# Kernel optimization log

Hardware: AMD Instinct MI355X
Metric: run time of the kernel (lower is better)

## Reference

```python
import jax, jax.numpy as jnp
import numpy as np

B, N, M, K = 8, 24000, 6000, 32
C_IN, C_MID, C_OUT = 64, 128, 256  # channels=[64,128,256]; conv input is C_IN+3 (dp_fj)


def setup_inputs() -> dict:
    key = jax.random.key(0)
    ks = jax.random.split(key, 8)
    return {
        "query_xyz": jax.random.normal(ks[0], (B, M, 3), jnp.float32),
        "support_xyz": jax.random.normal(ks[1], (B, N, 3), jnp.float32),
        "features": jax.random.normal(ks[2], (B, C_IN, N), jnp.float32),
        "neighbor_idx": jax.random.randint(ks[3], (B, M, K), 0, N, dtype=jnp.int32),
        "W1": jax.random.normal(ks[4], (C_MID, C_IN + 3), jnp.float32) * 0.05,
        "b1": jnp.zeros((C_MID,), jnp.float32),
        "W2": jax.random.normal(ks[5], (C_OUT, C_MID), jnp.float32) * 0.05,
        "b2": jnp.zeros((C_OUT,), jnp.float32),
    }


def _conv1d_relu(x, W, b):
    # pointwise conv1d (kernel size 1) + bias + ReLU; x: [B, Cin, N]
    return jax.nn.relu(jnp.einsum('oc,bcn->bon', W, x) + b[None, :, None])


def reference(query_xyz, support_xyz, features, neighbor_idx, W1, b1, W2, b2):
    # Delayed aggregation: transform features FIRST (convs on support points),
    # then gather neighbors per query and max-reduce.
    x = jnp.concatenate([features, support_xyz.transpose(0, 2, 1)], axis=1)  # [B, C_IN+3, N]
    x = _conv1d_relu(x, W1, b1)   # [B, C_MID, N]
    x = _conv1d_relu(x, W2, b2)   # [B, C_OUT, N]
    # grouper: gather neighbor features fj = x[b, :, neighbor_idx[b, m, k]] -> [B, C_OUT, M, K]
    idx = jnp.broadcast_to(neighbor_idx.reshape(B, 1, M * K), (B, C_OUT, M * K))
    fj = jnp.take_along_axis(x, idx, axis=2).reshape(B, C_OUT, M, K)
    # reduction_layer: max over neighbor dim
    return jnp.max(fj, axis=-1)  # [B, C_OUT, M]
```

## Files before the change

kernel.cpp:

```cpp
#include <hip/hip_runtime.h>

typedef unsigned short u16;
typedef short s16x8 __attribute__((ext_vector_type(8)));
typedef float f32x4 __attribute__((ext_vector_type(4)));
typedef unsigned short u16x8 __attribute__((ext_vector_type(8)));

#define B_   8
#define N_   24000
#define M_   6000
#define K_   32
#define CIN  64
#define CMID 128
#define COUT 256
#define KP1  96
#define QB_  188

__device__ __align__(16) u16 g_W1f[CMID * KP1];
__device__ __align__(16) u16 g_W2f[COUT * CMID];
__device__ __align__(16) u16 g_Yf[(size_t)B_ * N_ * COUT];

__device__ __forceinline__ float bf2f(u16 u) {
    return __uint_as_float(((unsigned)u) << 16);
}
__device__ __forceinline__ u16 f2bf(float f) {
    unsigned u = __float_as_uint(f);
    u += 0x7FFFu + ((u >> 16) & 1u);
    return (u16)(u >> 16);
}

__global__ void prep_weights(const float* __restrict__ W1,
                             const float* __restrict__ W2) {
    int t = blockIdx.x * 256 + threadIdx.x;
    if (t < CMID * KP1) {
        int blk = t >> 9, off = t & 511;
        int L = off >> 3, j = off & 7;
        int ln = L & 15, quad = L >> 4;
        int w = blk / 6, r = blk % 6;
        int k0i = r >> 1, mt = r & 1;
        int row = w * 32 + mt * 16 + ln;
        int col = k0i * 32 + quad * 8 + j;
        g_W1f[t] = (col < 67) ? f2bf(W1[row * 67 + col]) : (u16)0;
    } else {
        int i = t - CMID * KP1;
        int blk = i >> 9, off = i & 511;
        int L = off >> 3, j = off & 7;
        int ln = L & 15, quad = L >> 4;
        int w = blk >> 4, r = blk & 15;
        int k0i = r >> 2, mt = r & 3;
        int row = w * 64 + mt * 16 + ln;
        int col = k0i * 32 + quad * 8 + j;
        g_W2f[i] = f2bf(W2[row * 128 + col]);
    }
}

__global__ __launch_bounds__(256) void conv_fused(
        const float* __restrict__ feat, const float* __restrict__ xyz,
        const float* __restrict__ b1,  const float* __restrict__ b2) {
    __shared__ __align__(16) u16 sm[16896];
    u16* Xs = sm;
    u16* Hs = sm + 6656;
    u16* Ys = sm;

    const int tid  = threadIdx.x;
    const int b    = blockIdx.y;
    const int n0   = blockIdx.x * 64;
    const int w    = tid >> 6;
    const int L    = tid & 63;
    const int ln   = L & 15;
    const int quad = L >> 4;

    if (tid < 64) {
        uint4 z; z.x = z.y = z.z = z.w = 0u;
        u16* xr = Xs + tid * 104;
        *(uint4*)(xr + 64) = z; *(uint4*)(xr + 72) = z;
        *(uint4*)(xr + 80) = z; *(uint4*)(xr + 88) = z;
        const float* s = xyz + (size_t)(b * N_ + n0 + tid) * 3;
        xr[64] = f2bf(s[0]); xr[65] = f2bf(s[1]); xr[66] = f2bf(s[2]);
    }
#pragma unroll
    for (int it = 0; it < 4; ++it) {
        int idx = it * 256 + tid;
        int c   = idx >> 4;
        int p0  = (idx & 15) << 2;
        float4 v = *(const float4*)(feat + (size_t)(b * CIN + c) * N_ + n0 + p0);
        u16* dst = Xs + p0 * 104 + c;
        dst[0]   = f2bf(v.x);
        dst[104] = f2bf(v.y);
        dst[208] = f2bf(v.z);
        dst[312] = f2bf(v.w);
    }
    __syncthreads();

    f32x4 acc1[2][4];
#pragma unroll
    for (int mt = 0; mt < 2; ++mt)
#pragma unroll
        for (int nt = 0; nt < 4; ++nt) {
            f32x4 zz = {0.f, 0.f, 0.f, 0.f};
            acc1[mt][nt] = zz;
        }
#pragma unroll
    for (int k0i = 0; k0i < 3; ++k0i) {
        s16x8 af[2], xf[4];
#pragma unroll
        for (int mt = 0; mt < 2; ++mt)
            af[mt] = *(const s16x8*)(g_W1f + (((w * 3 + k0i) * 2 + mt) << 9) + L * 8);
#pragma unroll
        for (int nt = 0; nt < 4; ++nt)
            xf[nt] = *(const s16x8*)(Xs + (nt * 16 + ln) * 104 + k0i * 32 + quad * 8);
#pragma unroll
        for (int mt = 0; mt < 2; ++mt)
#pragma unroll
            for (int nt = 0; nt < 4; ++nt)
                acc1[mt][nt] = __builtin_amdgcn_mfma_f32_16x16x32_bf16(
                    af[mt], xf[nt], acc1[mt][nt], 0, 0, 0);
    }
#pragma unroll
    for (int mt = 0; mt < 2; ++mt) {
        int m0 = w * 32 + mt * 16 + quad * 4;
        float4 bv = *(const float4*)(b1 + m0);
#pragma unroll
        for (int nt = 0; nt < 4; ++nt) {
            int p = nt * 16 + ln;
            float x0 = acc1[mt][nt][0] + bv.x;
            float x1 = acc1[mt][nt][1] + bv.y;
            float x2 = acc1[mt][nt][2] + bv.z;
            float x3 = acc1[mt][nt][3] + bv.w;
            ushort4 hv;
            hv.x = f2bf(x0 > 0.f ? x0 : 0.f);
            hv.y = f2bf(x1 > 0.f ? x1 : 0.f);
            hv.z = f2bf(x2 > 0.f ? x2 : 0.f);
            hv.w = f2bf(x3 > 0.f ? x3 : 0.f);
            *(ushort4*)(Hs + p * 136 + m0) = hv;
        }
    }
    __syncthreads();

    f32x4 acc2[4][4];
#pragma unroll
    for (int mt = 0; mt < 4; ++mt)
#pragma unroll
        for (int nt = 0; nt < 4; ++nt) {
            f32x4 zz = {0.f, 0.f, 0.f, 0.f};
            acc2[mt][nt] = zz;
        }
#pragma unroll
    for (int k0i = 0; k0i < 4; ++k0i) {
        s16x8 af[4], hf[4];
#pragma unroll
        for (int mt = 0; mt < 4; ++mt)
            af[mt] = *(const s16x8*)(g_W2f + (((w * 4 + k0i) * 4 + mt) << 9) + L * 8);
#pragma unroll
        for (int nt = 0; nt < 4; ++nt)
            hf[nt] = *(const s16x8*)(Hs + (nt * 16 + ln) * 136 + k0i * 32 + quad * 8);
#pragma unroll
        for (int mt = 0; mt < 4; ++mt)
#pragma unroll
            for (int nt = 0; nt < 4; ++nt)
                acc2[mt][nt] = __builtin_amdgcn_mfma_f32_16x16x32_bf16(
                    af[mt], hf[nt], acc2[mt][nt], 0, 0, 0);
    }
    __syncthreads();

#pragma unroll
    for (int mt = 0; mt < 4; ++mt) {
        int c0 = w * 64 + mt * 16 + quad * 4;
        float4 bv = *(const float4*)(b2 + c0);
#pragma unroll
        for (int nt = 0; nt < 4; ++nt) {
            int p = nt * 16 + ln;
            float x0 = acc2[mt][nt][0] + bv.x;
            float x1 = acc2[mt][nt][1] + bv.y;
            float x2 = acc2[mt][nt][2] + bv.z;
            float x3 = acc2[mt][nt][3] + bv.w;
            ushort4 yv;
            yv.x = f2bf(x0 > 0.f ? x0 : 0.f);
            yv.y = f2bf(x1 > 0.f ? x1 : 0.f);
            yv.z = f2bf(x2 > 0.f ? x2 : 0.f);
            yv.w = f2bf(x3 > 0.f ? x3 : 0.f);
            *(ushort4*)(Ys + p * 264 + c0) = yv;
        }
    }
    __syncthreads();

    u16* dstY = g_Yf + ((size_t)b * N_ + n0) * COUT;
#pragma unroll
    for (int i = 0; i < 8; ++i) {
        int g = i * 256 + tid;
        int p = g >> 5, c16 = g & 31;
        *(uint4*)(dstY + (size_t)p * COUT + c16 * 8) =
            *(const uint4*)(Ys + p * 264 + c16 * 8);
    }
}

__global__ __launch_bounds__(256) void gather_max(
        const int* __restrict__ nbr, float* __restrict__ out) {
    __shared__ __align__(16) int sidx[32 * K_];
    __shared__ __align__(16) u16 ymax[32 * 400];

    const int tid = threadIdx.x;
    const int l   = blockIdx.x;
    const int xcd = l & 7;
    const int j   = l >> 3;
    const int cw  = j / QB_;
    const int qb  = j % QB_;
    const int combo = cw * 8 + xcd;
    const int b   = combo >> 2;
    const int q   = combo & 3;
    const int m0  = qb * 32;

    if (m0 + (tid >> 3) < M_)
        *(int4*)(sidx + tid * 4) =
            *(const int4*)(nbr + ((size_t)b * M_ + m0) * K_ + tid * 4);
    __syncthreads();

    const int w  = tid >> 6;
    const int L  = tid & 63;
    const int kg = L >> 3;
    const int co = L & 7;
    const u16* base = g_Yf + (size_t)b * N_ * COUT + q * 64 + co * 8;

    u16x8 mx[8];
#pragma unroll
    for (int i = 0; i < 8; ++i)
        mx[i] = (u16x8){0, 0, 0, 0, 0, 0, 0, 0};

#pragma unroll
    for (int nh = 0; nh < 2; ++nh) {
        const unsigned lo = nh ? (unsigned)(N_ / 2) : 0u;
        const unsigned hi = lo + (unsigned)(N_ / 2);
#pragma unroll
        for (int i = 0; i < 8; ++i) {
            int ml = w * 8 + i;
            if (m0 + ml < M_) {
                int id[4];
#pragma unroll
                for (int r = 0; r < 4; ++r)
                    id[r] = sidx[ml * K_ + r * 8 + kg];
                u16x8 v[4];
#pragma unroll
                for (int r = 0; r < 4; ++r) {
                    unsigned u = (unsigned)id[r];
                    u = u < (unsigned)N_ ? u : 0u;
                    if (u >= lo && u < hi)
                        v[r] = *(const u16x8*)(base + (size_t)u * COUT);
                    else
                        v[r] = (u16x8){0, 0, 0, 0, 0, 0, 0, 0};
                }
                u16x8 a = __builtin_elementwise_max(v[0], v[1]);
                u16x8 c = __builtin_elementwise_max(v[2], v[3]);
                mx[i] = __builtin_elementwise_max(
                    mx[i], __builtin_elementwise_max(a, c));
            }
        }
    }

#pragma unroll
    for (int i = 0; i < 8; ++i) {
        int ml = w * 8 + i;
        if (m0 + ml < M_) {
            u16x8 m8 = mx[i];
#pragma unroll
            for (int mask = 8; mask <= 32; mask <<= 1) {
                int4 t = *(int4*)&m8;
                t.x = __shfl_xor(t.x, mask);
                t.y = __shfl_xor(t.y, mask);
                t.z = __shfl_xor(t.z, mask);
                t.w = __shfl_xor(t.w, mask);
                m8 = __builtin_elementwise_max(m8, *(u16x8*)&t);
            }
            if (kg == 0)
                *(u16x8*)(ymax + ml * 400 + co * 8) = m8;
        }
    }
    __syncthreads();

    int valid = M_ - m0; if (valid > 32) valid = 32;
#pragma unroll
    for (int it = 0; it < 2; ++it) {
        int c  = it * 32 + (tid >> 3);
        int mc = (tid & 7) << 2;
        if (mc + 4 <= valid) {
            float4 v;
            v.x = bf2f(ymax[(mc + 0) * 400 + c]);
            v.y = bf2f(ymax[(mc + 1) * 400 + c]);
            v.z = bf2f(ymax[(mc + 2) * 400 + c]);
            v.w = bf2f(ymax[(mc + 3) * 400 + c]);
            *(float4*)(out + (size_t)(b * COUT + q * 64 + c) * M_ + m0 + mc) = v;
        }
    }
}

extern "C" void kernel_launch(void* const* d_in, const int* in_sizes, int n_in,
                              void* d_out, int out_size, void* d_ws, size_t ws_size,
                              hipStream_t stream) {
    const float* xyz  = (const float*)d_in[1];
    const float* feat = (const float*)d_in[2];
    const int*   nbr  = (const int*)d_in[3];
    const float* W1   = (const float*)d_in[4];
    const float* b1   = (const float*)d_in[5];
    const float* W2   = (const float*)d_in[6];
    const float* b2   = (const float*)d_in[7];
    float* out = (float*)d_out;
    (void)d_ws; (void)ws_size;

    prep_weights<<<176, 256, 0, stream>>>(W1, W2);
    conv_fused<<<dim3(N_ / 64, B_), 256, 0, stream>>>(feat, xyz, b1, b2);
    gather_max<<<32 * QB_, 256, 0, stream>>>(nbr, out);
}
```

Before: 257.0 us.

## Bucket neighbor indices by support-point range before gather to cut wasted loads

The gather kernel now counting-sorts each query's 32 neighbor indices in shared memory into three ranges of the support set (by idx>>13). It then loads features range by range, so each pass only touches an L2-sized slice of the feature table. Previously it made two masked passes over all indices and still issued loads for out-of-range entries. The change adds shared-memory atomics, extra barriers and a variable-length inner loop, and reuses one shared buffer for indices, sorted indices and the output staging.

```diff
diff --git a/kernel.cpp b/kernel.cpp
--- a/kernel.cpp
+++ b/kernel.cpp
@@ -195,8 +195,12 @@
 
 __global__ __launch_bounds__(256) void gather_max(
         const int* __restrict__ nbr, float* __restrict__ out) {
-    __shared__ __align__(16) int sidx[32 * K_];
-    __shared__ __align__(16) u16 ymax[32 * 400];
+    __shared__ __align__(16) u16 smem[32 * 400];
+    int* sidx  = (int*)smem;
+    u16* ssort = smem + 2048;
+    int* soff  = (int*)(smem + 3072);
+    int* scur  = (int*)(smem + 3328);
+    u16* ymax  = smem;
 
     const int tid = threadIdx.x;
     const int l   = blockIdx.x;
@@ -208,10 +212,45 @@
     const int b   = combo >> 2;
     const int q   = combo & 3;
     const int m0  = qb * 32;
-
-    if (m0 + (tid >> 3) < M_)
+    const int row = tid >> 3;
+    const int Mv0 = M_ - m0;
+    const int Mv  = Mv0 < 32 ? Mv0 : 32;
+
+    if (row < Mv)
         *(int4*)(sidx + tid * 4) =
             *(const int4*)(nbr + ((size_t)b * M_ + m0) * K_ + tid * 4);
+    if (tid < 128) scur[tid] = 0;
+    __syncthreads();
+
+    unsigned uu[4];
+#pragma unroll
+    for (int jj = 0; jj < 4; ++jj) {
+        unsigned u = (unsigned)sidx[tid * 4 + jj];
+        u = u < (unsigned)N_ ? u : 0u;
+        uu[jj] = u;
+        int p = (int)(u >> 13);
+        if (p < 2) atomicAdd(&scur[row * 4 + p], 1);
+    }
+    __syncthreads();
+
+    if (tid < 32) {
+        int c0 = scur[tid * 4 + 0], c1 = scur[tid * 4 + 1];
+        soff[tid * 4 + 0] = 0;
+        soff[tid * 4 + 1] = c0;
+        soff[tid * 4 + 2] = c0 + c1;
+        soff[tid * 4 + 3] = 32;
+        scur[tid * 4 + 0] = 0;
+        scur[tid * 4 + 1] = c0;
+        scur[tid * 4 + 2] = c0 + c1;
+    }
+    __syncthreads();
+
+#pragma unroll
+    for (int jj = 0; jj < 4; ++jj) {
+        int p = (int)(uu[jj] >> 13);
+        int pos = atomicAdd(&scur[row * 4 + p], 1);
+        ssort[row * 32 + pos] = (u16)uu[jj];
+    }
     __syncthreads();
 
     const int w  = tid >> 6;
@@ -226,39 +265,51 @@
         mx[i] = (u16x8){0, 0, 0, 0, 0, 0, 0, 0};
 
 #pragma unroll
-    for (int nh = 0; nh < 2; ++nh) {
-        const unsigned lo = nh ? (unsigned)(N_ / 2) : 0u;
-        const unsigned hi = lo + (unsigned)(N_ / 2);
-#pragma unroll
-        for (int i = 0; i < 8; ++i) {
-            int ml = w * 8 + i;
-            if (m0 + ml < M_) {
-                int id[4];
-#pragma unroll
-                for (int r = 0; r < 4; ++r)
-                    id[r] = sidx[ml * K_ + r * 8 + kg];
-                u16x8 v[4];
-#pragma unroll
-                for (int r = 0; r < 4; ++r) {
-                    unsigned u = (unsigned)id[r];
-                    u = u < (unsigned)N_ ? u : 0u;
-                    if (u >= lo && u < hi)
-                        v[r] = *(const u16x8*)(base + (size_t)u * COUT);
-                    else
-                        v[r] = (u16x8){0, 0, 0, 0, 0, 0, 0, 0};
+    for (int p = 0; p < 3; ++p) {
+#pragma unroll
+        for (int h = 0; h < 2; ++h) {
+            int mq[4], beg[4], end[4], last[4];
+            u16x8 va[4], vb[4];
+#pragma unroll
+            for (int s = 0; s < 4; ++s) {
+                int ml = w * 8 + h * 4 + s;
+                mq[s]  = ml < Mv ? ml : 0;
+                beg[s] = soff[mq[s] * 4 + p];
+                end[s] = soff[mq[s] * 4 + p + 1];
+                int lt = end[s] - 1;
+                last[s] = lt > 0 ? lt : 0;
+                int p0 = beg[s] + kg; p0 = p0 < last[s] ? p0 : last[s];
+                unsigned i0 = (unsigned)ssort[mq[s] * 32 + p0];
+                va[s] = *(const u16x8*)(base + (size_t)i0 * COUT);
+            }
+#pragma unroll
+            for (int s = 0; s < 4; ++s) {
+                int p1 = beg[s] + 8 + kg; p1 = p1 < last[s] ? p1 : last[s];
+                unsigned i1 = (unsigned)ssort[mq[s] * 32 + p1];
+                vb[s] = *(const u16x8*)(base + (size_t)i1 * COUT);
+            }
+#pragma unroll
+            for (int s = 0; s < 4; ++s)
+                mx[h * 4 + s] = __builtin_elementwise_max(mx[h * 4 + s],
+                    __builtin_elementwise_max(va[s], vb[s]));
+#pragma unroll
+            for (int s = 0; s < 4; ++s) {
+                for (int r = beg[s] + 16; r < end[s]; r += 8) {
+                    int pp = r + kg; pp = pp < last[s] ? pp : last[s];
+                    unsigned ii = (unsigned)ssort[mq[s] * 32 + pp];
+                    u16x8 vv = *(const u16x8*)(base + (size_t)ii * COUT);
+                    mx[h * 4 + s] = __builtin_elementwise_max(mx[h * 4 + s], vv);
                 }
-                u16x8 a = __builtin_elementwise_max(v[0], v[1]);
-                u16x8 c = __builtin_elementwise_max(v[2], v[3]);
-                mx[i] = __builtin_elementwise_max(
-                    mx[i], __builtin_elementwise_max(a, c));
             }
         }
     }
+
+    __syncthreads();
 
 #pragma unroll
     for (int i = 0; i < 8; ++i) {
         int ml = w * 8 + i;
-        if (m0 + ml < M_) {
+        if (ml < Mv) {
             u16x8 m8 = mx[i];
 #pragma unroll
             for (int mask = 8; mask <= 32; mask <<= 1) {
@@ -275,7 +326,7 @@
     }
     __syncthreads();
 
-    int valid = M_ - m0; if (valid > 32) valid = 32;
+    int valid = Mv;
 #pragma unroll
     for (int it = 0; it < 2; ++it) {
         int c  = it * 32 + (tid >> 3);
```

Result: no change. 255.8 us (-0.5%).

## Loop gather_max over four batch/channel combos per block and drop N-half split

Applied to the files above, without the earlier changes.

The gather_max grid shrinks 4x. Each block now iterates over four (batch, channel-quarter) combos within its XCD slot, reusing the block and aliasing the index and result shared buffers. The two-pass split over halves of N, which filtered indices by range and doubled the index reads and compares, is removed so each neighbor row is loaded once. Launch bounds now request 6 blocks per CU, which may limit registers. The extra barriers per iteration and fewer blocks could reduce latency hiding, and losing the N-half split may hurt L2 locality.

```diff
diff --git a/kernel.cpp b/kernel.cpp
--- a/kernel.cpp
+++ b/kernel.cpp
@@ -193,46 +193,48 @@
     }
 }
 
-__global__ __launch_bounds__(256) void gather_max(
+__global__ __launch_bounds__(256, 6) void gather_max(
         const int* __restrict__ nbr, float* __restrict__ out) {
-    __shared__ __align__(16) int sidx[32 * K_];
-    __shared__ __align__(16) u16 ymax[32 * 400];
+    __shared__ __align__(16) u16 smem[32 * 400];
+    int* sidx = (int*)smem;
+    u16* ymax = smem;
 
     const int tid = threadIdx.x;
     const int l   = blockIdx.x;
     const int xcd = l & 7;
-    const int j   = l >> 3;
-    const int cw  = j / QB_;
-    const int qb  = j % QB_;
-    const int combo = cw * 8 + xcd;
-    const int b   = combo >> 2;
-    const int q   = combo & 3;
+    const int qb  = l >> 3;
     const int m0  = qb * 32;
-
-    if (m0 + (tid >> 3) < M_)
-        *(int4*)(sidx + tid * 4) =
-            *(const int4*)(nbr + ((size_t)b * M_ + m0) * K_ + tid * 4);
-    __syncthreads();
+    const int row = tid >> 3;
+    const int Mv0 = M_ - m0;
+    const int Mv  = Mv0 < 32 ? Mv0 : 32;
 
     const int w  = tid >> 6;
     const int L  = tid & 63;
     const int kg = L >> 3;
     const int co = L & 7;
-    const u16* base = g_Yf + (size_t)b * N_ * COUT + q * 64 + co * 8;
-
-    u16x8 mx[8];
-#pragma unroll
-    for (int i = 0; i < 8; ++i)
-        mx[i] = (u16x8){0, 0, 0, 0, 0, 0, 0, 0};
-
-#pragma unroll
-    for (int nh = 0; nh < 2; ++nh) {
-        const unsigned lo = nh ? (unsigned)(N_ / 2) : 0u;
-        const unsigned hi = lo + (unsigned)(N_ / 2);
+
+    for (int cw = 0; cw < 4; ++cw) {
+        const int combo = cw * 8 + xcd;
+        const int b = combo >> 2;
+        const int q = combo & 3;
+
+        if (cw) __syncthreads();
+        if (row < Mv)
+            *(int4*)(sidx + tid * 4) =
+                *(const int4*)(nbr + ((size_t)b * M_ + m0) * K_ + tid * 4);
+        __syncthreads();
+
+        const u16* base = g_Yf + (size_t)b * N_ * COUT + q * 64 + co * 8;
+
+        u16x8 mx[8];
+#pragma unroll
+        for (int i = 0; i < 8; ++i)
+            mx[i] = (u16x8){0, 0, 0, 0, 0, 0, 0, 0};
+
 #pragma unroll
         for (int i = 0; i < 8; ++i) {
             int ml = w * 8 + i;
-            if (m0 + ml < M_) {
+            if (ml < Mv) {
                 int id[4];
 #pragma unroll
                 for (int r = 0; r < 4; ++r)
@@ -242,10 +244,7 @@
                 for (int r = 0; r < 4; ++r) {
                     unsigned u = (unsigned)id[r];
                     u = u < (unsigned)N_ ? u : 0u;
-                    if (u >= lo && u < hi)
-                        v[r] = *(const u16x8*)(base + (size_t)u * COUT);
-                    else
-                        v[r] = (u16x8){0, 0, 0, 0, 0, 0, 0, 0};
+                    v[r] = *(const u16x8*)(base + (size_t)u * COUT);
                 }
                 u16x8 a = __builtin_elementwise_max(v[0], v[1]);
                 u16x8 c = __builtin_elementwise_max(v[2], v[3]);
@@ -253,40 +252,40 @@
                     mx[i], __builtin_elementwise_max(a, c));
             }
         }
-    }
-
-#pragma unroll
-    for (int i = 0; i < 8; ++i) {
-        int ml = w * 8 + i;
-        if (m0 + ml < M_) {
-            u16x8 m8 = mx[i];
-#pragma unroll
-            for (int mask = 8; mask <= 32; mask <<= 1) {
-                int4 t = *(int4*)&m8;
-                t.x = __shfl_xor(t.x, mask);
-                t.y = __shfl_xor(t.y, mask);
-                t.z = __shfl_xor(t.z, mask);
-                t.w = __shfl_xor(t.w, mask);
-                m8 = __builtin_elementwise_max(m8, *(u16x8*)&t);
+        __syncthreads();
+
+#pragma unroll
+        for (int i = 0; i < 8; ++i) {
+            int ml = w * 8 + i;
+            if (ml < Mv) {
+                u16x8 m8 = mx[i];
+#pragma unroll
+                for (int mask = 8; mask <= 32; mask <<= 1) {
+                    int4 t = *(int4*)&m8;
+                    t.x = __shfl_xor(t.x, mask);
+                    t.y = __shfl_xor(t.y, mask);
+                    t.z = __shfl_xor(t.z, mask);
+                    t.w = __shfl_xor(t.w, mask);
+                    m8 = __builtin_elementwise_max(m8, *(u16x8*)&t);
+                }
+                if (kg == 0)
+                    *(u16x8*)(ymax + ml * 400 + co * 8) = m8;
             }
-            if (kg == 0)
-                *(u16x8*)(ymax + ml * 400 + co * 8) = m8;
-        }
-    }
-    __syncthreads();
-
-    int valid = M_ - m0; if (valid > 32) valid = 32;
-#pragma unroll
-    for (int it = 0; it < 2; ++it) {
-        int c  = it * 32 + (tid >> 3);
-        int mc = (tid & 7) << 2;
-        if (mc + 4 <= valid) {
-            float4 v;
-            v.x = bf2f(ymax[(mc + 0) * 400 + c]);
-            v.y = bf2f(ymax[(mc + 1) * 400 + c]);
-            v.z = bf2f(ymax[(mc + 2) * 400 + c]);
-            v.w = bf2f(ymax[(mc + 3) * 400 + c]);
-            *(float4*)(out + (size_t)(b * COUT + q * 64 + c) * M_ + m0 + mc) = v;
+        }
+        __syncthreads();
+
+#pragma unroll
+        for (int it = 0; it < 2; ++it) {
+            int c  = it * 32 + (tid >> 3);
+            int mc = (tid & 7) << 2;
+            if (mc + 4 <= Mv) {
+                float4 v;
+                v.x = bf2f(ymax[(mc + 0) * 400 + c]);
+                v.y = bf2f(ymax[(mc + 1) * 400 + c]);
+                v.z = bf2f(ymax[(mc + 2) * 400 + c]);
+                v.w = bf2f(ymax[(mc + 3) * 400 + c]);
+                *(float4*)(out + (size_t)(b * COUT + q * 64 + c) * M_ + m0 + mc) = v;
+            }
         }
     }
 }
@@ -306,5 +305,5 @@
 
     prep_weights<<<176, 256, 0, stream>>>(W1, W2);
     conv_fused<<<dim3(N_ / 64, B_), 256, 0, stream>>>(feat, xyz, b1, b2);
-    gather_max<<<32 * QB_, 256, 0, stream>>>(nbr, out);
-}
+    gather_max<<<8 * QB_, 256, 0, stream>>>(nbr, out);
+}
```

Result: slower. 304.8 us (+18.6%).
